# Kernel tuning notes

Hardware: AMD Instinct MI355X
Metric: run time of the kernel (lower is better)

The kernel has to match this reference:

```python
import jax, jax.numpy as jnp
import numpy as np

B, S, E, H = 4, 1024, 1024, 16
D = E // H          # head_dim = 64
F = 4 * E           # mlp inner = 4096
EPS = 1e-5


def _layernorm(x, scale, bias):
    mu = jnp.mean(x, axis=-1, keepdims=True)
    var = jnp.var(x, axis=-1, keepdims=True)
    return (x - mu) * jax.lax.rsqrt(var + EPS) * scale + bias


def setup_inputs() -> dict:
    key = jax.random.key(0)
    ks = jax.random.split(key, 8)
    std = 0.02
    return {
        "hidden_states": jax.random.normal(ks[0], (B, S, E), jnp.float32),
        "ln1_scale": jnp.ones((E,), jnp.float32),
        "ln1_bias": jnp.zeros((E,), jnp.float32),
        # Conv1D kernels stored as (out_features, in_features), applied as x @ k.T
        "w_attn": jax.random.normal(ks[1], (3 * E, E), jnp.float32) * std,
        "b_attn": jnp.zeros((3 * E,), jnp.float32),
        "w_proj": jax.random.normal(ks[2], (E, E), jnp.float32) * std,
        "b_proj": jnp.zeros((E,), jnp.float32),
        "ln2_scale": jnp.ones((E,), jnp.float32),
        "ln2_bias": jnp.zeros((E,), jnp.float32),
        "w_fc": jax.random.normal(ks[3], (F, E), jnp.float32) * std,
        "b_fc": jnp.zeros((F,), jnp.float32),
        "w_proj2": jax.random.normal(ks[4], (E, F), jnp.float32) * std,
        "b_proj2": jnp.zeros((E,), jnp.float32),
    }


def reference(hidden_states, ln1_scale, ln1_bias, w_attn, b_attn, w_proj, b_proj,
              ln2_scale, ln2_bias, w_fc, b_fc, w_proj2, b_proj2):
    x = hidden_states
    # --- attention sub-block ---
    h = _layernorm(x, ln1_scale, ln1_bias)
    qkv = h @ w_attn.T + b_attn                      # [B,S,3E]
    q, k, v = jnp.split(qkv, 3, axis=2)
    q = q.reshape(B, S, H, D) / jnp.sqrt(jnp.float32(D))
    k = k.reshape(B, S, H, D)
    v = v.reshape(B, S, H, D)
    # NOTE: source sets attention_bias = None, so NO causal mask is applied.
    logits = jnp.einsum("bqhd,bkhd->bhqk", q, k)     # [B,H,S,S]
    attn = jax.nn.softmax(logits, axis=-1)
    o = jnp.einsum("bhqk,bkhd->bqhd", attn, v).reshape(B, S, E)
    o = o @ w_proj.T + b_proj
    x = x + o
    # --- mlp sub-block ---
    h = _layernorm(x, ln2_scale, ln2_bias)
    m = jax.nn.gelu(h @ w_fc.T + b_fc, approximate=True)  # gelu_new
    m = m @ w_proj2.T + b_proj2
    return x + m
```

## Files before the change

### kernel.cpp

```cpp
#include <hip/hip_runtime.h>

#define DEV __device__ __forceinline__

using bf16x8 = __attribute__((ext_vector_type(8))) __bf16;
using f32x4  = __attribute__((ext_vector_type(4))) float;
typedef unsigned int u32;
typedef unsigned short u16;
typedef unsigned long long u64;

static constexpr int Bb = 4, Ss = 1024, Ee = 1024, Hh = 16, Dd = 64, Ff = 4096;
static constexpr int Mm = Bb * Ss;

DEV u16 f2bf(float f) {
  union { float f; u32 u; } v; v.f = f;
  u32 r = v.u + 0x7fffu + ((v.u >> 16) & 1u);
  return (u16)(r >> 16);
}

DEV void gload16(const void* g, void* lds) {
  __builtin_amdgcn_global_load_lds(
      (const __attribute__((address_space(1))) void*)(u64)g,
      (__attribute__((address_space(3))) void*)(u32)(u64)lds,
      16, 0, 0);
}

DEV float gelu_tanh(float x) {
  float x3 = x * x * x;
  float t  = tanhf(0.7978845608028654f * (x + 0.044715f * x3));
  return 0.5f * x * (1.0f + t);
}

DEV int swz(int row, int col) { return row * 64 + (col ^ ((row & 7) << 3)); }

DEV f32x4 MFMA(bf16x8 a, bf16x8 b, f32x4 c) {
  return __builtin_amdgcn_mfma_f32_16x16x32_bf16(a, b, c, 0, 0, 0);
}

__global__ __launch_bounds__(256) void cvt_bf16(const float* __restrict__ in,
                                                u16* __restrict__ out, int n) {
  int i = (blockIdx.x * 256 + threadIdx.x) * 8;
  if (i >= n) return;
  float4 a = *(const float4*)(in + i);
  float4 b = *(const float4*)(in + i + 4);
  uint4 o;
  o.x = (u32)f2bf(a.x) | ((u32)f2bf(a.y) << 16);
  o.y = (u32)f2bf(a.z) | ((u32)f2bf(a.w) << 16);
  o.z = (u32)f2bf(b.x) | ((u32)f2bf(b.y) << 16);
  o.w = (u32)f2bf(b.z) | ((u32)f2bf(b.w) << 16);
  *(uint4*)(out + i) = o;
}

__global__ __launch_bounds__(256) void ln_kernel(const float* __restrict__ x,
                                                 const float* __restrict__ scale,
                                                 const float* __restrict__ bias,
                                                 u16* __restrict__ h) {
  const int row = blockIdx.x, tid = threadIdx.x;
  const float4 v = ((const float4*)(x + (size_t)row * Ee))[tid];
  float s  = v.x + v.y + v.z + v.w;
  float ss = v.x * v.x + v.y * v.y + v.z * v.z + v.w * v.w;
  for (int m = 1; m < 64; m <<= 1) {
    s  += __shfl_xor(s, m, 64);
    ss += __shfl_xor(ss, m, 64);
  }
  __shared__ float red[8];
  const int w = tid >> 6, ln = tid & 63;
  if (ln == 0) { red[w * 2] = s; red[w * 2 + 1] = ss; }
  __syncthreads();
  s  = red[0] + red[2] + red[4] + red[6];
  ss = red[1] + red[3] + red[5] + red[7];
  const float mu   = s * (1.0f / Ee);
  const float var  = ss * (1.0f / Ee) - mu * mu;
  const float rstd = rsqrtf(var + 1e-5f);
  const float4 sc = ((const float4*)scale)[tid];
  const float4 bi = ((const float4*)bias)[tid];
  ushort4 o;
  o.x = f2bf((v.x - mu) * rstd * sc.x + bi.x);
  o.y = f2bf((v.y - mu) * rstd * sc.y + bi.y);
  o.z = f2bf((v.z - mu) * rstd * sc.z + bi.z);
  o.w = f2bf((v.w - mu) * rstd * sc.w + bi.w);
  ((ushort4*)(h + (size_t)row * Ee))[tid] = o;
}

template <int EPI>
__global__ __launch_bounds__(512, 2) void gemm8p(
    const u16* __restrict__ A, const u16* __restrict__ Bw,
    const float* __restrict__ bias,
    u16* __restrict__ outb,
    u16* __restrict__ q, u16* __restrict__ k, u16* __restrict__ v,
    int N, int K) {
  __shared__ u16 As8[2][256 * 64];
  __shared__ u16 Bs8[2][256 * 64];
  const int tid = threadIdx.x;
  const int w = tid >> 6, ln = tid & 63;
  const int lr = ln & 15, lg = ln >> 4;
  const int wr = w >> 2, wc = w & 3;

  const int nwg = gridDim.x * gridDim.y;
  const int bid = blockIdx.y * gridDim.x + blockIdx.x;
  const int sid = (bid & 7) * (nwg >> 3) + (bid >> 3);
  const int bx = sid % gridDim.x, by = sid / gridDim.x;
  const int tm = by * 256, tn = bx * 256;

  f32x4 acc[8][4];
  f32x4 zero4 = {0.f, 0.f, 0.f, 0.f};
#pragma unroll
  for (int i = 0; i < 8; ++i)
#pragma unroll
    for (int j = 0; j < 4; ++j) acc[i][j] = zero4;

  const int rA = tid >> 3;
  const int slv = (tid & 7) ^ (rA & 7);
  const u16* aS = A  + (size_t)(tm + rA) * K + (slv << 3);
  const u16* bS = Bw + (size_t)(tn + rA) * K + (slv << 3);
  const size_t g64 = (size_t)64 * K;

  auto STAGE = [&](int t) {
    const int c = t & 1;
    const int kc = t << 6;
#pragma unroll
    for (int g = 0; g < 4; ++g)
      gload16(aS + (size_t)g * g64 + kc, &As8[c][g * 4096 + tid * 8]);
#pragma unroll
    for (int g = 0; g < 4; ++g)
      gload16(bS + (size_t)g * g64 + kc, &Bs8[c][g * 4096 + tid * 8]);
  };

  const int sk0 = ((lg) ^ (lr & 7)) << 3;
  const int sk1 = ((4 | lg) ^ (lr & 7)) << 3;
  const int aBase = (wr * 128 + lr) * 64;
  const int bBase = (wc * 64 + lr) * 64;

  const int nkt = K >> 6;
  STAGE(0);
  STAGE(1);
  asm volatile("s_waitcnt vmcnt(8)" ::: "memory");
  __builtin_amdgcn_s_barrier();

  for (int kt = 0; kt < nkt; ++kt) {
    const u16* Ab = &As8[kt & 1][0];
    const u16* Bbuf = &Bs8[kt & 1][0];
    bf16x8 bfr[4][2];
#pragma unroll
    for (int n = 0; n < 4; ++n) {
      bfr[n][0] = *(const bf16x8*)&Bbuf[bBase + n * 1024 + sk0];
      bfr[n][1] = *(const bf16x8*)&Bbuf[bBase + n * 1024 + sk1];
    }
    __builtin_amdgcn_s_setprio(1);
#pragma unroll
    for (int ph = 0; ph < 4; ++ph) {
      bf16x8 a00 = *(const bf16x8*)&Ab[aBase + (2 * ph) * 1024 + sk0];
      bf16x8 a01 = *(const bf16x8*)&Ab[aBase + (2 * ph) * 1024 + sk1];
      bf16x8 a10 = *(const bf16x8*)&Ab[aBase + (2 * ph + 1) * 1024 + sk0];
      bf16x8 a11 = *(const bf16x8*)&Ab[aBase + (2 * ph + 1) * 1024 + sk1];
#pragma unroll
      for (int n = 0; n < 4; ++n) {
        acc[2 * ph][n]     = MFMA(a00, bfr[n][0], acc[2 * ph][n]);
        acc[2 * ph + 1][n] = MFMA(a10, bfr[n][0], acc[2 * ph + 1][n]);
        acc[2 * ph][n]     = MFMA(a01, bfr[n][1], acc[2 * ph][n]);
        acc[2 * ph + 1][n] = MFMA(a11, bfr[n][1], acc[2 * ph + 1][n]);
      }
    }
    __builtin_amdgcn_s_setprio(0);
    asm volatile("" ::: "memory");
    __builtin_amdgcn_s_barrier();
    if (kt + 2 < nkt) {
      STAGE(kt + 2);
      asm volatile("s_waitcnt vmcnt(8)" ::: "memory");
      __builtin_amdgcn_s_barrier();
    } else if (kt + 1 < nkt) {
      asm volatile("s_waitcnt vmcnt(0)" ::: "memory");
      __builtin_amdgcn_s_barrier();
    }
  }

#pragma unroll
  for (int mi = 0; mi < 8; ++mi) {
#pragma unroll
    for (int ni = 0; ni < 4; ++ni) {
      const int gc = tn + wc * 64 + ni * 16 + lr;
#pragma unroll
      for (int j = 0; j < 4; ++j) {
        const int gr = tm + wr * 128 + mi * 16 + lg * 4 + j;
        float val = acc[mi][ni][j] + bias[gc];
        if constexpr (EPI == 0) {
          const int which = gc >> 10, hh = (gc >> 6) & 15, dd = gc & 63;
          const int bb2 = gr >> 10, ss2 = gr & 1023;
          const size_t dst = ((size_t)(bb2 * 16 + hh) * 1024 + ss2) * 64 + dd;
          if (which == 0)      q[dst] = f2bf(val * 0.125f);
          else if (which == 1) k[dst] = f2bf(val);
          else                 v[dst] = f2bf(val);
        } else {
          outb[(size_t)gr * N + gc] = f2bf(gelu_tanh(val));
        }
      }
    }
  }
}

template <int EPI>
__global__ __launch_bounds__(256, 3) void gemm2(
    const u16* __restrict__ A, const u16* __restrict__ Bw,
    const float* __restrict__ bias, const float* __restrict__ resid,
    float* __restrict__ outf, u16* __restrict__ outb,
    u16* __restrict__ q, u16* __restrict__ k, u16* __restrict__ v,
    int N, int K) {
  __shared__ u16 As[3][128 * 32];
  __shared__ u16 Bs[3][128 * 32];
  const int tid = threadIdx.x;
  const int w = tid >> 6, ln = tid & 63;
  const int lr = ln & 15, lg = ln >> 4;

  const int nwg = gridDim.x * gridDim.y;
  const int bid = blockIdx.y * gridDim.x + blockIdx.x;
  const int sid = (bid & 7) * (nwg >> 3) + (bid >> 3);
  const int bx = sid % gridDim.x, by = sid / gridDim.x;
  const int tm = by * 128, tn = bx * 128;
  const int wr = (w >> 1) * 64, wc = (w & 1) * 64;

  f32x4 zero4 = {0.f, 0.f, 0.f, 0.f};
  f32x4 acc[4][4];
#pragma unroll
  for (int i = 0; i < 4; ++i)
#pragma unroll
    for (int j = 0; j < 4; ++j) acc[i][j] = zero4;

  const int r0 = tid >> 2, sl = tid & 3;
  const int cs = (sl ^ (r0 & 3)) * 8;
  const u16* aP0 = A  + (size_t)(tm + r0) * K + cs;
  const u16* aP1 = A  + (size_t)(tm + 64 + r0) * K + cs;
  const u16* bP0 = Bw + (size_t)(tn + r0) * K + cs;
  const u16* bP1 = Bw + (size_t)(tn + 64 + r0) * K + cs;

  auto STAGE = [&](int buf, int k0) {
    gload16(aP0 + k0, &As[buf][tid * 8]);
    gload16(aP1 + k0, &As[buf][(256 + tid) * 8]);
    gload16(bP0 + k0, &Bs[buf][tid * 8]);
    gload16(bP1 + k0, &Bs[buf][(256 + tid) * 8]);
  };

  const int nt = K >> 5;
  STAGE(0, 0);
  STAGE(1, 32);
  asm volatile("s_waitcnt vmcnt(4)" ::: "memory");
  __builtin_amdgcn_s_barrier();
  __builtin_amdgcn_sched_barrier(0);

  for (int t = 0; t < nt; ++t) {
    const int cur = t % 3;
    const bool more = (t + 2) < nt;
    if (more) STAGE((t + 2) % 3, (t + 2) << 5);

    bf16x8 af[4], bb[4];
#pragma unroll
    for (int mi = 0; mi < 4; ++mi) {
      const int row = wr + mi * 16 + lr;
      af[mi] = *(const bf16x8*)&As[cur][row * 32 + ((lg ^ (row & 3)) << 3)];
    }
#pragma unroll
    for (int ni = 0; ni < 4; ++ni) {
      const int row = wc + ni * 16 + lr;
      bb[ni] = *(const bf16x8*)&Bs[cur][row * 32 + ((lg ^ (row & 3)) << 3)];
    }
    __builtin_amdgcn_s_setprio(1);
#pragma unroll
    for (int mi = 0; mi < 4; ++mi)
#pragma unroll
      for (int ni = 0; ni < 4; ++ni)
        acc[mi][ni] = MFMA(af[mi], bb[ni], acc[mi][ni]);
    __builtin_amdgcn_s_setprio(0);
    __builtin_amdgcn_sched_barrier(0);
    if (more) asm volatile("s_waitcnt vmcnt(4)" ::: "memory");
    else      asm volatile("s_waitcnt vmcnt(0)" ::: "memory");
    __builtin_amdgcn_s_barrier();
    __builtin_amdgcn_sched_barrier(0);
  }

#pragma unroll
  for (int mi = 0; mi < 4; ++mi) {
#pragma unroll
    for (int ni = 0; ni < 4; ++ni) {
      const int gc = tn + wc + ni * 16 + lr;
#pragma unroll
      for (int j = 0; j < 4; ++j) {
        const int gr = tm + wr + mi * 16 + lg * 4 + j;
        float val = acc[mi][ni][j] + bias[gc];
        if constexpr (EPI == 1) {
          const size_t idx = (size_t)gr * N + gc;
          outf[idx] = val + resid[idx];
        } else {
          outb[(size_t)gr * N + gc] = f2bf(gelu_tanh(val));
        }
      }
    }
  }
}

__global__ __launch_bounds__(256) void attn_kernel(const u16* __restrict__ qg,
                                                   const u16* __restrict__ kg,
                                                   const u16* __restrict__ vg,
                                                   u16* __restrict__ ao) {
  __shared__ u16 Qs[64 * 64], Ks[64 * 64], Vt[64 * 64], Ps[64 * 64];
  const int tid = threadIdx.x;
  const int w = tid >> 6, ln = tid & 63;
  const int lr = ln & 15, lg = ln >> 4;
  const int bh = blockIdx.y;
  const int q0 = blockIdx.x * 64;
  const size_t head = (size_t)bh * (Ss * Dd);

  {
    const u16* src = qg + head + (size_t)q0 * Dd;
#pragma unroll
    for (int i = 0; i < 2; ++i) {
      const int gi = i * 256 + tid, row = gi >> 3, g = gi & 7;
      *(uint4*)&Qs[row * 64 + ((g ^ (row & 7)) << 3)] = *(const uint4*)(src + gi * 8);
    }
  }

  f32x4 zero4 = {0.f, 0.f, 0.f, 0.f};
  f32x4 acc_o[4] = {zero4, zero4, zero4, zero4};
  float mrow[4] = {-1e30f, -1e30f, -1e30f, -1e30f};
  float lrow[4] = {0.f, 0.f, 0.f, 0.f};

  for (int kt = 0; kt < 16; ++kt) {
    __syncthreads();
    const u16* ksrc = kg + head + (size_t)kt * 64 * Dd;
    const u16* vsrc = vg + head + (size_t)kt * 64 * Dd;
#pragma unroll
    for (int i = 0; i < 2; ++i) {
      const int gi = i * 256 + tid, row = gi >> 3, g = gi & 7;
      *(uint4*)&Ks[row * 64 + ((g ^ (row & 7)) << 3)] = *(const uint4*)(ksrc + gi * 8);
    }
#pragma unroll
    for (int i = 0; i < 2; ++i) {
      const int kv = i * 32 + (tid >> 3), d0 = (tid & 7) * 8;
      uint4 dv = *(const uint4*)(vsrc + (size_t)kv * Dd + d0);
      const u16* pv = (const u16*)&dv;
#pragma unroll
      for (int j = 0; j < 8; ++j) {
        const int dd = d0 + j;
        Vt[dd * 64 + (((kv >> 3) ^ (dd & 7)) << 3) + (kv & 7)] = pv[j];
      }
    }
    __syncthreads();

    bf16x8 aq[2];
#pragma unroll
    for (int kk = 0; kk < 2; ++kk)
      aq[kk] = *(const bf16x8*)&Qs[swz(w * 16 + lr, kk * 32 + lg * 8)];
    f32x4 sa[4];
#pragma unroll
    for (int kf = 0; kf < 4; ++kf) {
      f32x4 s = zero4;
#pragma unroll
      for (int kk = 0; kk < 2; ++kk) {
        bf16x8 bk = *(const bf16x8*)&Ks[swz(kf * 16 + lr, kk * 32 + lg * 8)];
        s = MFMA(aq[kk], bk, s);
      }
      sa[kf] = s;
    }

#pragma unroll
    for (int j = 0; j < 4; ++j) {
      float mx = fmaxf(fmaxf(sa[0][j], sa[1][j]), fmaxf(sa[2][j], sa[3][j]));
      mx = fmaxf(mx, __shfl_xor(mx, 1, 64));
      mx = fmaxf(mx, __shfl_xor(mx, 2, 64));
      mx = fmaxf(mx, __shfl_xor(mx, 4, 64));
      mx = fmaxf(mx, __shfl_xor(mx, 8, 64));
      const float nm = fmaxf(mrow[j], mx);
      const float corr = __expf(mrow[j] - nm);
      mrow[j] = nm;
      float ssum = 0.f;
#pragma unroll
      for (int kf = 0; kf < 4; ++kf) {
        const float p = __expf(sa[kf][j] - nm);
        sa[kf][j] = p;
        ssum += p;
      }
      ssum += __shfl_xor(ssum, 1, 64);
      ssum += __shfl_xor(ssum, 2, 64);
      ssum += __shfl_xor(ssum, 4, 64);
      ssum += __shfl_xor(ssum, 8, 64);
      lrow[j] = lrow[j] * corr + ssum;
#pragma unroll
      for (int df = 0; df < 4; ++df) acc_o[df][j] *= corr;
    }

#pragma unroll
    for (int kf = 0; kf < 4; ++kf)
#pragma unroll
      for (int j = 0; j < 4; ++j)
        Ps[swz(w * 16 + lg * 4 + j, kf * 16 + lr)] = f2bf(sa[kf][j]);

    __syncthreads();

    bf16x8 ap[2];
#pragma unroll
    for (int kk = 0; kk < 2; ++kk)
      ap[kk] = *(const bf16x8*)&Ps[swz(w * 16 + lr, kk * 32 + lg * 8)];
#pragma unroll
    for (int df = 0; df < 4; ++df) {
#pragma unroll
      for (int kk = 0; kk < 2; ++kk) {
        bf16x8 bv = *(const bf16x8*)&Vt[swz(df * 16 + lr, kk * 32 + lg * 8)];
        acc_o[df] = MFMA(ap[kk], bv, acc_o[df]);
      }
    }
  }

  const int b = bh >> 4, h = bh & 15;
#pragma unroll
  for (int df = 0; df < 4; ++df) {
#pragma unroll
    for (int j = 0; j < 4; ++j) {
      const int srow = q0 + w * 16 + lg * 4 + j;
      const int e = h * 64 + df * 16 + lr;
      ao[((size_t)b * Ss + srow) * Ee + e] = f2bf(acc_o[df][j] / lrow[j]);
    }
  }
}

extern "C" void kernel_launch(void* const* d_in, const int* in_sizes, int n_in,
                              void* d_out, int out_size, void* d_ws, size_t ws_size,
                              hipStream_t stream) {
  const float* x      = (const float*)d_in[0];
  const float* ln1_s  = (const float*)d_in[1];
  const float* ln1_b  = (const float*)d_in[2];
  const float* w_attn = (const float*)d_in[3];
  const float* b_attn = (const float*)d_in[4];
  const float* w_proj = (const float*)d_in[5];
  const float* b_proj = (const float*)d_in[6];
  const float* ln2_s  = (const float*)d_in[7];
  const float* ln2_b  = (const float*)d_in[8];
  const float* w_fc   = (const float*)d_in[9];
  const float* b_fc   = (const float*)d_in[10];
  const float* w_proj2= (const float*)d_in[11];
  const float* b_proj2= (const float*)d_in[12];
  float* out = (float*)d_out;

  char* base = (char*)d_ws;
  size_t off = 0;
  auto alloc = [&](size_t bytes) { char* p = base + off; off += bytes; return p; };
  u16* wA   = (u16*)alloc((size_t)3 * Ee * Ee * 2);
  u16* wP   = (u16*)alloc((size_t)Ee * Ee * 2);
  u16* wF   = (u16*)alloc((size_t)Ff * Ee * 2);
  u16* wP2  = (u16*)alloc((size_t)Ee * Ff * 2);
  u16* h1   = (u16*)alloc((size_t)Mm * Ee * 2);
  u16* qws  = (u16*)alloc((size_t)Mm * Ee * 2);
  u16* kws  = (u16*)alloc((size_t)Mm * Ee * 2);
  u16* vws  = (u16*)alloc((size_t)Mm * Ee * 2);
  u16* aws  = (u16*)alloc((size_t)Mm * Ee * 2);
  float* x1 = (float*)alloc((size_t)Mm * Ee * 4);
  u16* mfc  = qws;

  cvt_bf16<<<3 * Ee * Ee / 2048, 256, 0, stream>>>(w_attn, wA, 3 * Ee * Ee);
  cvt_bf16<<<Ee * Ee / 2048, 256, 0, stream>>>(w_proj, wP, Ee * Ee);
  cvt_bf16<<<Ff * Ee / 2048, 256, 0, stream>>>(w_fc, wF, Ff * Ee);
  cvt_bf16<<<Ee * Ff / 2048, 256, 0, stream>>>(w_proj2, wP2, Ee * Ff);

  ln_kernel<<<Mm, 256, 0, stream>>>(x, ln1_s, ln1_b, h1);
  gemm8p<0><<<dim3(12, 16), 512, 0, stream>>>(h1, wA, b_attn,
                                              nullptr, qws, kws, vws,
                                              3 * Ee, Ee);
  attn_kernel<<<dim3(16, 64), 256, 0, stream>>>(qws, kws, vws, aws);
  gemm2<1><<<dim3(8, 32), 256, 0, stream>>>(aws, wP, b_proj, x,
                                            x1, nullptr, nullptr, nullptr, nullptr,
                                            Ee, Ee);
  ln_kernel<<<Mm, 256, 0, stream>>>(x1, ln2_s, ln2_b, h1);
  gemm8p<2><<<dim3(16, 16), 512, 0, stream>>>(h1, wF, b_fc,
                                              mfc, nullptr, nullptr, nullptr,
                                              Ff, Ee);
  gemm2<1><<<dim3(8, 32), 256, 0, stream>>>(mfc, wP2, b_proj2, x1,
                                            out, nullptr, nullptr, nullptr, nullptr,
                                            Ee, Ff);
}
```

Measured before the change: 316.9 us.

## Restructure GEMM main loop into four-phase pipeline with split K-half LDS buffers

The GEMM LDS tiles are split into two K=32 halves per buffer, and each K=64 iteration becomes four phases. Each phase reads A/B fragments, issues one quarter of the next tile's global-to-LDS loads, then runs 16 MFMAs. Interleaving the loads at finer granularity is meant to spread memory traffic across the compute so the MFMA units are not left waiting at a single staging barrier. The trade-off is more barriers and explicit waitcnt/sched_barrier ordering per iteration, which could add sync overhead or expose LDS latency.

```diff
diff --git a/kernel.cpp b/kernel.cpp
--- a/kernel.cpp
+++ b/kernel.cpp
@@ -88,8 +88,8 @@
     u16* __restrict__ outb,
     u16* __restrict__ q, u16* __restrict__ k, u16* __restrict__ v,
     int N, int K) {
-  __shared__ u16 As8[2][256 * 64];
-  __shared__ u16 Bs8[2][256 * 64];
+  __shared__ u16 AS[2][2][256 * 32];
+  __shared__ u16 BS[2][2][256 * 32];
   const int tid = threadIdx.x;
   const int w = tid >> 6, ln = tid & 63;
   const int lr = ln & 15, lg = ln >> 4;
@@ -108,69 +108,91 @@
 #pragma unroll
     for (int j = 0; j < 4; ++j) acc[i][j] = zero4;
 
-  const int rA = tid >> 3;
-  const int slv = (tid & 7) ^ (rA & 7);
-  const u16* aS = A  + (size_t)(tm + rA) * K + (slv << 3);
-  const u16* bS = Bw + (size_t)(tn + rA) * K + (slv << 3);
-  const size_t g64 = (size_t)64 * K;
-
-  auto STAGE = [&](int t) {
-    const int c = t & 1;
-    const int kc = t << 6;
-#pragma unroll
-    for (int g = 0; g < 4; ++g)
-      gload16(aS + (size_t)g * g64 + kc, &As8[c][g * 4096 + tid * 8]);
-#pragma unroll
-    for (int g = 0; g < 4; ++g)
-      gload16(bS + (size_t)g * g64 + kc, &Bs8[c][g * 4096 + tid * 8]);
-  };
-
-  const int sk0 = ((lg) ^ (lr & 7)) << 3;
-  const int sk1 = ((4 | lg) ^ (lr & 7)) << 3;
-  const int aBase = (wr * 128 + lr) * 64;
-  const int bBase = (wc * 64 + lr) * 64;
+  const int srow = tid >> 2;
+  const int gsl  = (tid & 3) ^ (srow & 3);
+  const u16* aG = A  + (size_t)(tm + srow) * K + gsl * 8;
+  const u16* bG = Bw + (size_t)(tn + srow) * K + gsl * 8;
+
+  auto STG = [&](u16* lds, const u16* g, int koff) {
+    gload16(g + koff, lds + tid * 8);
+    gload16(g + (size_t)128 * K + koff, lds + 4096 + tid * 8);
+  };
+
+  const int fsl = (lg ^ (lr & 3)) << 3;
+  const int aRow = wr * 128 + lr;
+  const int bRow = wc * 64 + lr;
+
+  auto RD_A = [&](bf16x8* dst, const u16* half, int mh) {
+#pragma unroll
+    for (int i = 0; i < 4; ++i)
+      dst[i] = *(const bf16x8*)&half[(aRow + (mh * 4 + i) * 16) * 32 + fsl];
+  };
+  auto RD_B = [&](bf16x8* dst, const u16* half) {
+#pragma unroll
+    for (int i = 0; i < 4; ++i)
+      dst[i] = *(const bf16x8*)&half[(bRow + i * 16) * 32 + fsl];
+  };
+  auto MF16 = [&](int mh, const bf16x8* a, const bf16x8* b) {
+    __builtin_amdgcn_s_setprio(1);
+#pragma unroll
+    for (int i = 0; i < 4; ++i)
+#pragma unroll
+      for (int n = 0; n < 4; ++n)
+        acc[mh * 4 + i][n] = MFMA(a[i], b[n], acc[mh * 4 + i][n]);
+    __builtin_amdgcn_s_setprio(0);
+  };
+  auto BAR = [&]() { __builtin_amdgcn_s_barrier(); };
+  auto LGKM0 = [&]() {
+    asm volatile("s_waitcnt lgkmcnt(0)" ::: "memory");
+    __builtin_amdgcn_sched_barrier(0);
+  };
 
   const int nkt = K >> 6;
-  STAGE(0);
-  STAGE(1);
-  asm volatile("s_waitcnt vmcnt(8)" ::: "memory");
-  __builtin_amdgcn_s_barrier();
-
-  for (int kt = 0; kt < nkt; ++kt) {
-    const u16* Ab = &As8[kt & 1][0];
-    const u16* Bbuf = &Bs8[kt & 1][0];
-    bf16x8 bfr[4][2];
-#pragma unroll
-    for (int n = 0; n < 4; ++n) {
-      bfr[n][0] = *(const bf16x8*)&Bbuf[bBase + n * 1024 + sk0];
-      bfr[n][1] = *(const bf16x8*)&Bbuf[bBase + n * 1024 + sk1];
-    }
-    __builtin_amdgcn_s_setprio(1);
-#pragma unroll
-    for (int ph = 0; ph < 4; ++ph) {
-      bf16x8 a00 = *(const bf16x8*)&Ab[aBase + (2 * ph) * 1024 + sk0];
-      bf16x8 a01 = *(const bf16x8*)&Ab[aBase + (2 * ph) * 1024 + sk1];
-      bf16x8 a10 = *(const bf16x8*)&Ab[aBase + (2 * ph + 1) * 1024 + sk0];
-      bf16x8 a11 = *(const bf16x8*)&Ab[aBase + (2 * ph + 1) * 1024 + sk1];
-#pragma unroll
-      for (int n = 0; n < 4; ++n) {
-        acc[2 * ph][n]     = MFMA(a00, bfr[n][0], acc[2 * ph][n]);
-        acc[2 * ph + 1][n] = MFMA(a10, bfr[n][0], acc[2 * ph + 1][n]);
-        acc[2 * ph][n]     = MFMA(a01, bfr[n][1], acc[2 * ph][n]);
-        acc[2 * ph + 1][n] = MFMA(a11, bfr[n][1], acc[2 * ph + 1][n]);
-      }
-    }
-    __builtin_amdgcn_s_setprio(0);
-    asm volatile("" ::: "memory");
-    __builtin_amdgcn_s_barrier();
-    if (kt + 2 < nkt) {
-      STAGE(kt + 2);
-      asm volatile("s_waitcnt vmcnt(8)" ::: "memory");
-      __builtin_amdgcn_s_barrier();
-    } else if (kt + 1 < nkt) {
-      asm volatile("s_waitcnt vmcnt(0)" ::: "memory");
-      __builtin_amdgcn_s_barrier();
-    }
+  STG(&AS[0][0][0], aG, 0);
+  STG(&BS[0][0][0], bG, 0);
+  STG(&AS[0][1][0], aG, 32);
+  STG(&BS[0][1][0], bG, 32);
+  asm volatile("s_waitcnt vmcnt(4)" ::: "memory");
+  BAR();
+
+  for (int t = 0; t < nkt; ++t) {
+    const int c = t & 1, nc = c ^ 1;
+    const u16* A0 = &AS[c][0][0];
+    const u16* A1 = &AS[c][1][0];
+    const u16* B0 = &BS[c][0][0];
+    const u16* B1 = &BS[c][1][0];
+    const bool more = (t + 1) < nkt;
+    const int koff = (t + 1) << 6;
+    bf16x8 a[4], bk0[4], bk1[4];
+
+    RD_A(a, A0, 0);
+    RD_B(bk0, B0);
+    if (more) STG(&AS[nc][0][0], aG, koff);
+    BAR(); LGKM0();
+    MF16(0, a, bk0);
+    BAR();
+
+    RD_A(a, A0, 1);
+    if (more) STG(&BS[nc][0][0], bG, koff);
+    BAR(); LGKM0();
+    MF16(1, a, bk0);
+    if (more) asm volatile("s_waitcnt vmcnt(4)" ::: "memory");
+    else      asm volatile("s_waitcnt vmcnt(0)" ::: "memory");
+    BAR();
+
+    RD_A(a, A1, 0);
+    RD_B(bk1, B1);
+    if (more) STG(&AS[nc][1][0], aG, koff + 32);
+    BAR(); LGKM0();
+    MF16(0, a, bk1);
+    BAR();
+
+    RD_A(a, A1, 1);
+    if (more) STG(&BS[nc][1][0], bG, koff + 32);
+    BAR(); LGKM0();
+    MF16(1, a, bk1);
+    if (more) asm volatile("s_waitcnt vmcnt(4)" ::: "memory");
+    BAR();
   }
 
 #pragma unroll
```

Measured after the change: 322.2 us. No clear change (+1.7%).
